# Kernel tuning notes

Hardware: AMD Instinct MI355X
Metric: run time of the kernel (lower is better)

Reference implementation:

```python
import jax, jax.numpy as jnp
import numpy as np

H = 8          # query heads
HKV = 4        # kv heads
D = 256        # head dim
GROUPS = H // HKV
HIDDEN = 2304
WINDOW = 2048  # sliding window
SOFTCAP = 50.0
SCALE = (HIDDEN // H) ** -0.5  # query_pre_attn_scalar uses hidden//heads, not head_dim
NEG = -1e9
ROPE_BASE = 10000.0


def _rope_tables(L, offset=0, dtype=jnp.float32):
    inv_freq = 1.0 / (ROPE_BASE ** (jnp.arange(0, D, 2, dtype=jnp.float32) / D))
    t = jnp.arange(offset, offset + L, dtype=jnp.float32)
    freqs = jnp.outer(t, inv_freq)                    # [L, D/2]
    emb = jnp.concatenate([freqs, freqs], axis=-1)    # [L, D]
    return jnp.cos(emb).astype(dtype), jnp.sin(emb).astype(dtype)


def _rotate_half(x):
    x1, x2 = jnp.split(x, 2, axis=-1)
    return jnp.concatenate([-x2, x1], axis=-1)


def _apply_rope(x, cos, sin):
    # x: [B, h, L, D]; cos/sin: [L, D]
    return x * cos[None, None] + _rotate_half(x) * sin[None, None]


def setup_inputs() -> dict:
    key = jax.random.key(0)
    ks = jax.random.split(key, 5)
    B, L = 1, 4096
    x = jax.random.normal(ks[0], (B, L, HIDDEN), dtype=jnp.float32)
    wq = jax.random.normal(ks[1], (HIDDEN, H * D), dtype=jnp.float32) * 0.02
    wk = jax.random.normal(ks[2], (HIDDEN, HKV * D), dtype=jnp.float32) * 0.02
    wv = jax.random.normal(ks[3], (HIDDEN, HKV * D), dtype=jnp.float32) * 0.02
    wo = jax.random.normal(ks[4], (H * D, HIDDEN), dtype=jnp.float32) * 0.02
    # additive causal mask [1,1,L,L]
    causal = jnp.triu(jnp.full((L, L), NEG, dtype=jnp.float32), k=1)
    mask = causal[None, None]
    return {"x": x, "mask": mask, "wq": wq, "wk": wk, "wv": wv, "wo": wo}


def reference(x, mask, wq, wk, wv, wo):
    B, L, _ = x.shape
    q = (x @ wq).reshape(B, L, H, D).transpose(0, 2, 1, 3)     # [B,H,L,D]
    k = (x @ wk).reshape(B, L, HKV, D).transpose(0, 2, 1, 3)   # [B,HKV,L,D]
    v = (x @ wv).reshape(B, L, HKV, D).transpose(0, 2, 1, 3)

    cos, sin = _rope_tables(L, 0, q.dtype)
    q = _apply_rope(q, cos, sin)
    k = _apply_rope(k, cos, sin)

    # GQA: repeat_interleave kv heads
    k = jnp.repeat(k, GROUPS, axis=1)  # [B,H,L,D]
    v = jnp.repeat(v, GROUPS, axis=1)

    attn = jnp.einsum("bhqd,bhkd->bhqk", q, k) * SCALE
    attn = SOFTCAP * jnp.tanh(attn / SOFTCAP)
    attn = attn + mask

    kv_len = attn.shape[-1]
    if kv_len > WINDOW:  # sliding branch: keep only last WINDOW key columns
        col_keep = jnp.arange(kv_len) >= (kv_len - WINDOW)  # [kv_len]
        attn = jnp.where(col_keep[None, None, None, :], attn, NEG)

    attn = jax.nn.softmax(attn.astype(jnp.float32), axis=-1).astype(q.dtype)
    out = jnp.einsum("bhqk,bhkd->bhqd", attn, v)
    out = out.transpose(0, 2, 1, 3).reshape(B, L, H * D)
    return out @ wo
```

## Files before the change

kernel.cpp:

```cpp
#include <hip/hip_runtime.h>

typedef unsigned short u16;
typedef __bf16 bf16x8 __attribute__((ext_vector_type(8)));
typedef float floatx4 __attribute__((ext_vector_type(4)));
typedef unsigned short u16x4 __attribute__((ext_vector_type(4)));
typedef unsigned short u16x8 __attribute__((ext_vector_type(8)));

#define L_SEQ 4096
#define HID   2304
#define NH    8
#define NKV   4
#define HD    256
#define QDIM  2048
#define KVDIM 1024
#define SCALE_F 0.05892556509887896f

__device__ __forceinline__ u16 f2bf(float f) {
  unsigned u = __float_as_uint(f);
  u += 0x7FFFu + ((u >> 16) & 1u);
  return (u16)(u >> 16);
}
__device__ __forceinline__ float bf2f(u16 h) {
  return __uint_as_float(((unsigned)h) << 16);
}

__device__ __forceinline__ void async_load16(const u16* g, u16* lds_base) {
  __builtin_amdgcn_global_load_lds(
      (const __attribute__((address_space(1))) unsigned int*)g,
      (__attribute__((address_space(3))) unsigned int*)lds_base, 16, 0, 0);
}

__global__ __launch_bounds__(256)
void transpose_kernel(const float* __restrict__ wq, const float* __restrict__ wk,
                      const float* __restrict__ wv, const float* __restrict__ wo,
                      const float* __restrict__ x,
                      u16* __restrict__ wqkvT, u16* __restrict__ woT,
                      u16* __restrict__ xb) {
  const int z = blockIdx.z;
  if (z == 4) {
    const int n4 = L_SEQ * HID / 4;
    const int bid = blockIdx.y * 72 + blockIdx.x;
    const int stride = 5184 * 256;
#pragma unroll
    for (int k = 0; k < 2; ++k) {
      const int i = bid * 256 + threadIdx.x + k * stride;
      if (i < n4) {
        float4 v = *reinterpret_cast<const float4*>(&x[(size_t)i * 4]);
        u16x4 o;
        o[0] = f2bf(v.x); o[1] = f2bf(v.y); o[2] = f2bf(v.z); o[3] = f2bf(v.w);
        *reinterpret_cast<u16x4*>(&xb[(size_t)i * 4]) = o;
      }
    }
    return;
  }
  const float* W; u16* WT; int K, N;
  if (z == 0)      { W = wq; WT = wqkvT;                            K = HID;  N = QDIM; }
  else if (z == 1) { W = wk; WT = wqkvT + (size_t)QDIM * HID;       K = HID;  N = KVDIM; }
  else if (z == 2) { W = wv; WT = wqkvT + (size_t)(QDIM + KVDIM) * HID; K = HID; N = KVDIM; }
  else             { W = wo; WT = woT;                              K = QDIM; N = HID; }
  const int n0 = blockIdx.x * 32, k0 = blockIdx.y * 32;
  if (n0 >= N || k0 >= K) return;
  __shared__ u16 t[32][33];
  const int c = threadIdx.x & 31, r4 = (threadIdx.x >> 5) * 4;
#pragma unroll
  for (int i = 0; i < 4; ++i)
    t[r4 + i][c] = f2bf(W[(size_t)(k0 + r4 + i) * N + n0 + c]);
  __syncthreads();
  const int nn = threadIdx.x & 31, kb = (threadIdx.x >> 5) * 4;
  u16x4 o;
#pragma unroll
  for (int j = 0; j < 4; ++j) o[j] = t[kb + j][nn];
  *reinterpret_cast<u16x4*>(&WT[(size_t)(n0 + nn) * K + k0 + kb]) = o;
}

#define G256_NT 36

#define G256_BARRIER() __builtin_amdgcn_s_barrier()
#define G256_SCHEDB()  __builtin_amdgcn_sched_barrier(0)

#define G256_STAGE(bb, X, kh, tt)                                              \
  {                                                                            \
    const u16* g = (X) ? BT + (size_t)(n0 + w * 32 + srow) * HID               \
                       : A + (size_t)(m0 + w * 32 + srow) * HID;               \
    const int kc = (tt) * 64 + (kh) * 32 + schk;                               \
    async_load16(g + kc, &lds[bb][X][kh][(w * 32) * 32]);                      \
    async_load16(g + 16 * HID + kc, &lds[bb][X][kh][(w * 32 + 16) * 32]);      \
  }

#define G256_RD_B(dst, bb, kk)                                                 \
  {                                                                            \
    const u16* Bk = &lds[bb][1][kk][0];                                        \
    _Pragma("unroll") for (int nt = 0; nt < 4; ++nt)                           \
        dst[nt] = *reinterpret_cast<const bf16x8*>(                            \
            &Bk[(wn + nt * 16 + l16) * 32 + rsw]);                             \
  }

#define G256_RD_A(dst, bb, kk, ch)                                             \
  {                                                                            \
    const u16* Ak = &lds[bb][0][kk][0];                                        \
    _Pragma("unroll") for (int mt = 0; mt < 4; ++mt)                           \
        dst[mt] = *reinterpret_cast<const bf16x8*>(                            \
            &Ak[(wm + ((ch) * 4 + mt) * 16 + l16) * 32 + rsw]);                \
  }

#define G256_MFMA(ch, AA, BB)                                                  \
  {                                                                            \
    __builtin_amdgcn_s_setprio(1);                                             \
    _Pragma("unroll") for (int mt = 0; mt < 4; ++mt)                           \
        _Pragma("unroll") for (int nt = 0; nt < 4; ++nt)                       \
            acc[(ch) * 4 + mt][nt] = __builtin_amdgcn_mfma_f32_16x16x32_bf16(  \
                AA[mt], BB[nt], acc[(ch) * 4 + mt][nt], 0, 0, 0);              \
    __builtin_amdgcn_s_setprio(0);                                             \
  }

#define G256_VMCNT4() __asm__ volatile("s_waitcnt vmcnt(4)")
#define G256_VMCNT0() __asm__ volatile("s_waitcnt vmcnt(0)")

__global__ __launch_bounds__(512)
void gemm256_kernel(const u16* __restrict__ A, const u16* __restrict__ BT,
                    u16* __restrict__ C) {
  __shared__ __align__(16) u16 lds[2][2][2][256 * 32];

  const int tid  = threadIdx.x;
  const int lane = tid & 63;
  const int w    = tid >> 6;
  const int l16  = lane & 15;
  const int quad = lane >> 4;
  const int wm   = (w >> 2) * 128;
  const int wn   = (w & 3) * 64;

  const int srow = lane >> 2;
  const int schk = (((lane & 3) ^ ((lane >> 3) & 3))) * 8;
  const int rsw = ((quad ^ ((l16 >> 1) & 3))) * 8;

  const int bid = blockIdx.x;
  const int id  = (bid & 7) * 20 + (bid >> 3);

  int m0, n0, region;
  if (id < 64)      { region = 0; n0 = (id & 7) * 256;          m0 = 2048 + (id >> 3) * 256; }
  else if (id < 96) { region = 1; const int i = id - 64;
                      n0 = 2048 + (i & 3) * 256;                m0 = 2048 + (i >> 2) * 256; }
  else              { region = 2; const int i = id - 96;
                      n0 = 3072 + (i & 3) * 256;                m0 = (i >> 2) * 256; }

  floatx4 acc[8][4];
#pragma unroll
  for (int i = 0; i < 8; ++i)
#pragma unroll
    for (int j = 0; j < 4; ++j) acc[i][j] = (floatx4){0.f, 0.f, 0.f, 0.f};

  G256_STAGE(0, 0, 0, 0); G256_STAGE(0, 1, 0, 0);
  G256_STAGE(0, 0, 1, 0); G256_STAGE(0, 1, 1, 0);
  G256_STAGE(1, 0, 0, 1); G256_STAGE(1, 1, 0, 1);
  G256_VMCNT4();
  G256_BARRIER();

#pragma unroll 2
  for (int t = 0; t < G256_NT; ++t) {
    const int bb = t & 1;
    bf16x8 a_cur[4], b_cur[4], a_hi0[4], a_lo1[4], b1[4], a_hi1[4];

    G256_RD_A(a_cur, bb, 0, 0);
    G256_RD_B(b_cur, bb, 0);
    G256_RD_A(a_hi0, bb, 0, 1);
    if (t + 1 < G256_NT) { G256_STAGE(bb ^ 1, 0, 1, t + 1); }
    G256_SCHEDB();
    G256_MFMA(0, a_cur, b_cur);
    G256_BARRIER();

    G256_RD_A(a_lo1, bb, 1, 0);
    G256_RD_B(b1, bb, 1);
    if (t + 1 < G256_NT) { G256_STAGE(bb ^ 1, 1, 1, t + 1); }
    G256_SCHEDB();
    G256_MFMA(1, a_hi0, b_cur);
    G256_BARRIER();

    G256_RD_A(a_hi1, bb, 1, 1);
    if (t + 2 < G256_NT) { G256_STAGE(bb, 0, 0, t + 2); }
    G256_SCHEDB();
    G256_MFMA(0, a_lo1, b1);
    G256_BARRIER();

    if (t + 2 < G256_NT) { G256_STAGE(bb, 1, 0, t + 2); }
    G256_SCHEDB();
    G256_MFMA(1, a_hi1, b1);
    if (t < G256_NT - 2) { G256_VMCNT4(); }
    else                 { G256_VMCNT0(); }
    G256_BARRIER();
  }

#pragma unroll
  for (int mt = 0; mt < 8; ++mt)
#pragma unroll
    for (int nt = 0; nt < 4; ++nt) {
      const int mbase = m0 + wm + mt * 16 + quad * 4;
      const int n = n0 + wn + nt * 16 + l16;
      if (region == 0) {
        const size_t base = (size_t)(n >> 8) * L_SEQ * HD + (n & 255);
#pragma unroll
        for (int r = 0; r < 4; ++r)
          C[base + (size_t)(mbase + r) * HD] = f2bf(acc[mt][nt][r] * SCALE_F);
      } else if (region == 1) {
        const int nk2 = n - QDIM;
        const size_t base = (size_t)NH * L_SEQ * HD +
                            (size_t)(nk2 >> 8) * L_SEQ * HD + (nk2 & 255);
#pragma unroll
        for (int r = 0; r < 4; ++r)
          C[base + (size_t)(mbase + r) * HD] = f2bf(acc[mt][nt][r]);
      } else {
        const int nv = n - QDIM - KVDIM;
        u16x4 o;
#pragma unroll
        for (int r = 0; r < 4; ++r) o[r] = f2bf(acc[mt][nt][r]);
        *reinterpret_cast<u16x4*>(
            &C[(size_t)(NH + NKV) * L_SEQ * HD +
               ((size_t)(nv >> 8) * HD + (nv & 255)) * L_SEQ + mbase]) = o;
      }
    }
}

#define GOUT_NT 32

#define GP_STAGE(KS, bb, X, kh, tt)                                            \
  {                                                                            \
    const u16* g = (X) ? BT + (size_t)(n0 + w * 32 + srow) * (KS)              \
                       : A + (size_t)(m0 + w * 32 + srow) * (KS);              \
    const int kc = (tt) * 64 + (kh) * 32 + schk;                               \
    async_load16(g + kc, &lds[bb][X][kh][(w * 32) * 32]);                      \
    async_load16(g + 16 * (KS) + kc, &lds[bb][X][kh][(w * 32 + 16) * 32]);     \
  }

#define GP_RD(dstA, dstB, bb, kk)                                              \
  {                                                                            \
    const u16* Ak = &lds[bb][0][kk][0];                                        \
    const u16* Bk = &lds[bb][1][kk][0];                                        \
    _Pragma("unroll") for (int mt = 0; mt < 4; ++mt)                           \
        dstA[mt] = *reinterpret_cast<const bf16x8*>(                           \
            &Ak[(wm + mt * 16 + l16) * 32 + rsw]);                             \
    _Pragma("unroll") for (int nt = 0; nt < 4; ++nt)                           \
        dstB[nt] = *reinterpret_cast<const bf16x8*>(                           \
            &Bk[(wn + nt * 16 + l16) * 32 + rsw]);                             \
  }

#define GP_MFMA(AA, BB)                                                        \
  {                                                                            \
    __builtin_amdgcn_s_setprio(1);                                             \
    _Pragma("unroll") for (int mt = 0; mt < 4; ++mt)                           \
        _Pragma("unroll") for (int nt = 0; nt < 4; ++nt)                       \
            acc[mt][nt] = __builtin_amdgcn_mfma_f32_16x16x32_bf16(             \
                AA[mt], BB[nt], acc[mt][nt], 0, 0, 0);                         \
    __builtin_amdgcn_s_setprio(0);                                             \
  }

__global__ __launch_bounds__(256)
void gemm_out_kernel(const u16* __restrict__ A, const u16* __restrict__ BT,
                     float* __restrict__ C, const float* __restrict__ rvec,
                     float* __restrict__ out_lo) {
  __shared__ __align__(16) u16 lds[2][2][2][128 * 32];

  const int bid = blockIdx.x;
  const int id  = (bid & 7) * 45 + (bid >> 3);

  if (id >= 288) {
    const int b = id - 288;
    const int total = 2048 * 576;
    for (int i = b * 256 + threadIdx.x; i < total; i += 72 * 256) {
      const int col4 = i % 576;
      *reinterpret_cast<float4*>(&out_lo[(size_t)i * 4]) =
          *reinterpret_cast<const float4*>(&rvec[col4 * 4]);
    }
    return;
  }

  const int tid  = threadIdx.x;
  const int lane = tid & 63;
  const int w    = tid >> 6;
  const int l16  = lane & 15;
  const int quad = lane >> 4;
  const int wm   = (w >> 1) * 64;
  const int wn   = (w & 1) * 64;

  const int srow = lane >> 2;
  const int schk = (((lane & 3) ^ ((lane >> 3) & 3))) * 8;
  const int rsw  = ((quad ^ ((l16 >> 1) & 3))) * 8;

  const int n0  = (id % 18) * 128;
  const int m0  = (id / 18) * 128;

  floatx4 acc[4][4];
#pragma unroll
  for (int i = 0; i < 4; ++i)
#pragma unroll
    for (int j = 0; j < 4; ++j) acc[i][j] = (floatx4){0.f, 0.f, 0.f, 0.f};

  GP_STAGE(QDIM, 0, 0, 0, 0); GP_STAGE(QDIM, 0, 1, 0, 0);
  GP_STAGE(QDIM, 0, 0, 1, 0); GP_STAGE(QDIM, 0, 1, 1, 0);
  GP_STAGE(QDIM, 1, 0, 0, 1); GP_STAGE(QDIM, 1, 1, 0, 1);
  G256_VMCNT4();
  G256_BARRIER();

#pragma unroll 2
  for (int t = 0; t < GOUT_NT; ++t) {
    const int bb = t & 1;
    bf16x8 a0[4], b0[4], a1[4], b1[4];

    GP_RD(a0, b0, bb, 0);
    GP_RD(a1, b1, bb, 1);
    if (t + 1 < GOUT_NT) { GP_STAGE(QDIM, bb ^ 1, 0, 1, t + 1);
                           GP_STAGE(QDIM, bb ^ 1, 1, 1, t + 1); }
    G256_SCHEDB();
    GP_MFMA(a0, b0);
    G256_BARRIER();

    if (t + 2 < GOUT_NT) { GP_STAGE(QDIM, bb, 0, 0, t + 2);
                           GP_STAGE(QDIM, bb, 1, 0, t + 2); }
    G256_SCHEDB();
    GP_MFMA(a1, b1);
    if (t < GOUT_NT - 2) { G256_VMCNT4(); }
    else                 { G256_VMCNT0(); }
    G256_BARRIER();
  }

#pragma unroll
  for (int mt = 0; mt < 4; ++mt)
#pragma unroll
    for (int nt = 0; nt < 4; ++nt) {
      const int mbase = m0 + wm + mt * 16 + quad * 4;
      const int n = n0 + wn + nt * 16 + l16;
#pragma unroll
      for (int r = 0; r < 4; ++r)
        C[(size_t)(mbase + r) * HID + n] = acc[mt][nt][r];
    }
}

__global__ __launch_bounds__(384)
void rope_meanv_kernel(u16* __restrict__ qb, u16* __restrict__ kb,
                       const u16* __restrict__ vt, float* __restrict__ mv) {
  if (blockIdx.x >= 2048) {
    if (threadIdx.x >= 256) return;
    const int row  = (blockIdx.x - 2048) * 4 + (threadIdx.x >> 6);
    const int lane = threadIdx.x & 63;
    const u16* p = vt + (size_t)row * L_SEQ;
    float s = 0.f;
#pragma unroll
    for (int c = 0; c < 8; ++c) {
      u16x8 v = *reinterpret_cast<const u16x8*>(&p[(c * 64 + lane) * 8]);
#pragma unroll
      for (int j = 0; j < 8; ++j) s += bf2f(v[j]);
    }
#pragma unroll
    for (int off = 32; off > 0; off >>= 1) s += __shfl_xor(s, off, 64);
    if (lane == 0) mv[row] = s * (1.0f / 4096.0f);
    return;
  }
  const int l  = 2048 + blockIdx.x;
  const int hh = threadIdx.x >> 5;
  const int d0 = (threadIdx.x & 31) * 4;
  u16* base = (hh < NH) ? qb + ((size_t)hh * L_SEQ + l) * HD
                        : kb + ((size_t)(hh - NH) * L_SEQ + l) * HD;
  u16x4 x1v = *reinterpret_cast<const u16x4*>(&base[d0]);
  u16x4 x2v = *reinterpret_cast<const u16x4*>(&base[d0 + 128]);
  u16x4 o1, o2;
#pragma unroll
  for (int i = 0; i < 4; ++i) {
    const float invf = exp2f((float)(d0 + i) * (-13.287712379549449f / 128.0f));
    const float ang = (float)l * invf;
    float s, c;
    sincosf(ang, &s, &c);
    const float x1 = bf2f(x1v[i]);
    const float x2 = bf2f(x2v[i]);
    o1[i] = f2bf(x1 * c - x2 * s);
    o2[i] = f2bf(x2 * c + x1 * s);
  }
  *reinterpret_cast<u16x4*>(&base[d0])       = o1;
  *reinterpret_cast<u16x4*>(&base[d0 + 128]) = o2;
}

__global__ __launch_bounds__(256)
void rowvec_part_kernel(const float* __restrict__ mv, const float* __restrict__ wo,
                        float* __restrict__ rpart) {
  const int j = blockIdx.x * 256 + threadIdx.x;
  const int c0 = blockIdx.y * 128;
  float acc = 0.f;
#pragma unroll 4
  for (int cc = 0; cc < 128; ++cc) {
    const int c = c0 + cc;
    const float a = mv[((c >> 9) << 8) | (c & 255)];
    acc += a * wo[(size_t)c * HID + j];
  }
  rpart[blockIdx.y * HID + j] = acc;
}

__global__ __launch_bounds__(256)
void rowvec_reduce_kernel(const float* __restrict__ rpart, float* __restrict__ r) {
  const int j = blockIdx.x * 256 + threadIdx.x;
  float s = 0.f;
#pragma unroll
  for (int p = 0; p < 16; ++p) s += rpart[p * HID + j];
  r[j] = s;
}

#define ATT_STAGE(g_, buf_)                                                    \
  {                                                                            \
    const int kt_ = r_off[run] + (g_);                                         \
    const u16* kg_ = kg0 + (size_t)kt_ * 32 * HD;                              \
    _Pragma("unroll") for (int p_ = 0; p_ < 4; ++p_) {                         \
      const int r_   = w * 8 + p_ * 2 + (lane >> 5);                           \
      const int pos_ = lane & 31;                                              \
      const int c_   = (pos_ & 24) | ((pos_ ^ r_) & 7);                        \
      async_load16(&kg_[(size_t)r_ * HD + c_ * 8],                             \
                   &Klds[buf_][(w * 8 + p_ * 2) * 256]);                       \
    }                                                                          \
    const u16* vg_ = vg0 + kt_ * 32;                                           \
    _Pragma("unroll") for (int j_ = 0; j_ < 4; ++j_) {                         \
      const int m_  = w * 32 + j_ * 8 + (lane >> 3);                           \
      const int p2_ = lane & 7;                                                \
      const int c2_ = p2_ ^ (m_ & 7);                                          \
      const int r2_ = m_ * 2 + (c2_ >> 2);                                     \
      async_load16(&vg_[(size_t)r2_ * L_SEQ + (c2_ & 3) * 8],                  \
                   &Vlds[buf_][(w * 32 + j_ * 8) * 64]);                       \
    }                                                                          \
  }

__global__ __launch_bounds__(256)
void attn_kernel(const u16* __restrict__ qb, const u16* __restrict__ kb,
                 const u16* __restrict__ vt, u16* __restrict__ Opart,
                 float* __restrict__ lpart) {
  const int s = blockIdx.x;
  const int pr = blockIdx.y;
  const int h = blockIdx.z;
  const int kvh = h >> 1;
  const int tid = threadIdx.x;
  const int w = tid >> 6, lane = tid & 63;
  const int l16 = lane & 15, quad = lane >> 4;

  __shared__ __align__(16) u16 Klds[2][32 * 256];
  __shared__ __align__(16) u16 Vlds[2][256 * 32];
  __shared__ u16 Plds[4][16][40];

  const int n_a = 2 * pr + 2;
  const int lo = (66 * s) >> 2;
  const int hi = (66 * (s + 1)) >> 2;

  const int r_lo[2] = {lo, (lo > n_a) ? lo : n_a};
  const int r_hi[2] = {(hi < n_a) ? hi : n_a, hi};
  const int r_t[2]  = {32 + pr, 63 - pr};
  const int r_off[2] = {64, 64 - n_a};

  const u16* kg0 = kb + (size_t)kvh * L_SEQ * HD;
  const u16* vg0 = vt + (size_t)kvh * HD * L_SEQ;

  for (int run = 0; run < 2; ++run) {
    if (r_lo[run] >= r_hi[run]) continue;
    const int t  = r_t[run];
    const int q0 = t * 64 + w * 16;
    const int glo = r_lo[run], ghi = r_hi[run];

    bf16x8 aq[8];
    {
      const u16* qr = qb + ((size_t)h * L_SEQ + q0 + l16) * HD + quad * 8;
#pragma unroll
      for (int f = 0; f < 8; ++f)
        aq[f] = *reinterpret_cast<const bf16x8*>(&qr[f * 32]);
#pragma unroll
      for (int f = 0; f < 8; ++f) {
        floatx4& t4 = reinterpret_cast<floatx4&>(aq[f]);
        __asm__ volatile("" : "+v"(t4));
      }
    }

    ATT_STAGE(glo, 0);
    if (glo + 1 < ghi) ATT_STAGE(glo + 1, 1);

    floatx4 acc[16];
#pragma unroll
    for (int i = 0; i < 16; ++i) acc[i] = (floatx4){0.f, 0.f, 0.f, 0.f};
    float lsum[4] = {0.f, 0.f, 0.f, 0.f};

    for (int g = glo; g < ghi; ++g) {
      const int cur = (g - glo) & 1;
      const int kt = r_off[run] + g;
      if (g + 1 < ghi) { __asm__ volatile("s_waitcnt vmcnt(8)"); }
      else             { __asm__ volatile("s_waitcnt vmcnt(0)"); }
      __builtin_amdgcn_s_barrier();

      const u16* Kb = &Klds[cur][0];
      const u16* Vb = &Vlds[cur][0];

      floatx4 sa[2] = {(floatx4){0.f, 0.f, 0.f, 0.f}, (floatx4){0.f, 0.f, 0.f, 0.f}};
#pragma unroll
      for (int nt = 0; nt < 2; ++nt) {
        const int row = nt * 16 + l16;
#pragma unroll
        for (int f = 0; f < 8; ++f) {
          const int c   = f * 4 + quad;
          const int pos = (c & 24) | ((c ^ row) & 7);
          bf16x8 bk = *reinterpret_cast<const bf16x8*>(&Kb[row * 256 + pos * 8]);
          sa[nt] = __builtin_amdgcn_mfma_f32_16x16x32_bf16(aq[f], bk, sa[nt], 0, 0, 0);
        }
      }
#pragma unroll
      for (int nt = 0; nt < 2; ++nt) {
        const int key = kt * 32 + nt * 16 + l16;
#pragma unroll
        for (int r = 0; r < 4; ++r) {
          const float x = sa[nt][r];
          const float capm50 = -100.0f / (__expf(x * 0.04f) + 1.0f);
          float p = __expf(capm50);
          const int qq = q0 + quad * 4 + r;
          p = (key <= qq) ? p : 0.0f;
          lsum[r] += p;
          Plds[w][quad * 4 + r][nt * 16 + l16] = f2bf(p);
        }
      }
      bf16x8 ap = *reinterpret_cast<const bf16x8*>(&Plds[w][l16][quad * 8]);
#pragma unroll
      for (int dt = 0; dt < 16; ++dt) {
        const int rV = dt * 16 + l16;
        const int m  = rV >> 1;
        const int p  = ((rV & 1) * 4 + quad) ^ (m & 7);
        bf16x8 bv = *reinterpret_cast<const bf16x8*>(&Vb[m * 64 + p * 8]);
        acc[dt] = __builtin_amdgcn_mfma_f32_16x16x32_bf16(ap, bv, acc[dt], 0, 0, 0);
      }

      __builtin_amdgcn_s_barrier();
      if (g + 2 < ghi) ATT_STAGE(g + 2, cur);
    }

#pragma unroll
    for (int r = 0; r < 4; ++r) {
      float l = lsum[r];
      l += __shfl_xor(l, 1); l += __shfl_xor(l, 2);
      l += __shfl_xor(l, 4); l += __shfl_xor(l, 8);
      lsum[r] = l;
    }
    const int ql0 = q0 - 2048 + quad * 4;
#pragma unroll
    for (int r = 0; r < 4; ++r) {
      u16* orow = Opart + (((size_t)s * NH + h) * 2048 + ql0 + r) * HD + l16;
#pragma unroll
      for (int dt = 0; dt < 16; ++dt) orow[dt * 16] = f2bf(acc[dt][r]);
      if (l16 == 0) lpart[((size_t)s * NH + h) * 2048 + ql0 + r] = lsum[r];
    }
  }
}

__global__ __launch_bounds__(256)
void combine_kernel(const u16* __restrict__ Opart, const float* __restrict__ lpart,
                    u16* __restrict__ ab) {
  const int idx4 = blockIdx.x * 256 + threadIdx.x;
  const int d4 = (idx4 & 63) * 4;
  const int ql = (idx4 >> 6) & 2047;
  const int h  = idx4 >> 17;
  const int qtile = ql >> 6;
  const bool role_a = qtile < 16;
  const int pr = role_a ? qtile : 31 - qtile;
  const int lo_s[4] = {0, 16, 33, 49};
  const int hi_s[4] = {16, 33, 49, 66};

  float4 o = {0.f, 0.f, 0.f, 0.f};
  float l = 0.f;
#pragma unroll
  for (int s = 0; s < 4; ++s) {
    const bool valid = role_a ? (lo_s[s] < 2 * pr + 2) : (hi_s[s] > 2 * pr + 2);
    if (valid) {
      u16x4 v = *reinterpret_cast<const u16x4*>(
          &Opart[(((size_t)s * NH + h) * 2048 + ql) * HD + d4]);
      o.x += bf2f(v[0]); o.y += bf2f(v[1]); o.z += bf2f(v[2]); o.w += bf2f(v[3]);
      l += lpart[((size_t)s * NH + h) * 2048 + ql];
    }
  }
  const float inv = 1.0f / l;
  u16x4 ov;
  ov[0] = f2bf(o.x * inv); ov[1] = f2bf(o.y * inv);
  ov[2] = f2bf(o.z * inv); ov[3] = f2bf(o.w * inv);
  *reinterpret_cast<u16x4*>(&ab[(size_t)(2048 + ql) * QDIM + h * HD + d4]) = ov;
}

extern "C" void kernel_launch(void* const* d_in, const int* in_sizes, int n_in,
                              void* d_out, int out_size, void* d_ws, size_t ws_size,
                              hipStream_t stream) {
  const float* x  = (const float*)d_in[0];
  const float* wq = (const float*)d_in[2];
  const float* wk = (const float*)d_in[3];
  const float* wv = (const float*)d_in[4];
  const float* wo = (const float*)d_in[5];
  float* out = (float*)d_out;

  u16* qb  = (u16*)d_ws;
  u16* kb  = qb  + (size_t)NH  * L_SEQ * HD;
  u16* vtb = kb  + (size_t)NKV * L_SEQ * HD;
  u16* ab  = vtb + (size_t)NKV * L_SEQ * HD;
  u16* xb  = ab  + (size_t)L_SEQ * QDIM;
  u16* wqkvT = xb + (size_t)L_SEQ * HID;
  u16* woT = wqkvT + (size_t)(QDIM + 2 * KVDIM) * HID;
  u16* Opart = woT + (size_t)HID * QDIM;
  float* lpart = (float*)(Opart + (size_t)4 * NH * 2048 * HD);
  float* mv    = lpart + (size_t)4 * NH * 2048;
  float* rpart = mv + 1024;
  float* rvec  = rpart + 16 * HID;

  transpose_kernel<<<dim3(72, 72, 5), 256, 0, stream>>>(
      wq, wk, wv, wo, x, wqkvT, woT, xb);

  gemm256_kernel<<<dim3(160), 512, 0, stream>>>(xb, wqkvT, qb);

  rope_meanv_kernel<<<dim3(2048 + 256), 384, 0, stream>>>(qb, kb, vtb, mv);

  rowvec_part_kernel<<<dim3(9, 16), 256, 0, stream>>>(mv, wo, rpart);
  rowvec_reduce_kernel<<<dim3(9), 256, 0, stream>>>(rpart, rvec);

  attn_kernel<<<dim3(4, 16, NH), 256, 0, stream>>>(qb, kb, vtb, Opart, lpart);
  combine_kernel<<<dim3(4096), 256, 0, stream>>>(Opart, lpart, ab);

  gemm_out_kernel<<<dim3(360), 256, 0, stream>>>(
      ab + (size_t)2048 * QDIM, woT, out + (size_t)2048 * HID, rvec, out);
}
```

Before: 328.6 us.

## Single-buffer V in LDS and split attention work into six KV chunks

V tiles now go into a single LDS buffer, loaded right after the compute barrier, while K stays double-buffered. This cuts LDS per block so more blocks can be resident. The KV range per pair is now split into six chunks of 11 tiles instead of four, giving 768 blocks instead of 512 for better CU fill. The cost is exposed V load latency, more partial outputs written to workspace, and more reads in the combine kernel.

```diff
diff --git a/kernel.cpp b/kernel.cpp
--- a/kernel.cpp
+++ b/kernel.cpp
@@ -400,7 +400,7 @@
   r[j] = s;
 }
 
-#define ATT_STAGE(g_, buf_)                                                    \
+#define ATT_STAGE_K(g_, buf_)                                                  \
   {                                                                            \
     const int kt_ = r_off[run] + (g_);                                         \
     const u16* kg_ = kg0 + (size_t)kt_ * 32 * HD;                              \
@@ -411,6 +411,11 @@
       async_load16(&kg_[(size_t)r_ * HD + c_ * 8],                             \
                    &Klds[buf_][(w * 8 + p_ * 2) * 256]);                       \
     }                                                                          \
+  }
+
+#define ATT_STAGE_V(g_)                                                        \
+  {                                                                            \
+    const int kt_ = r_off[run] + (g_);                                         \
     const u16* vg_ = vg0 + kt_ * 32;                                           \
     _Pragma("unroll") for (int j_ = 0; j_ < 4; ++j_) {                         \
       const int m_  = w * 32 + j_ * 8 + (lane >> 3);                           \
@@ -418,7 +423,7 @@
       const int c2_ = p2_ ^ (m_ & 7);                                          \
       const int r2_ = m_ * 2 + (c2_ >> 2);                                     \
       async_load16(&vg_[(size_t)r2_ * L_SEQ + (c2_ & 3) * 8],                  \
-                   &Vlds[buf_][(w * 32 + j_ * 8) * 64]);                       \
+                   &Vlds[(w * 32 + j_ * 8) * 64]);                             \
     }                                                                          \
   }
 
@@ -435,12 +440,12 @@
   const int l16 = lane & 15, quad = lane >> 4;
 
   __shared__ __align__(16) u16 Klds[2][32 * 256];
-  __shared__ __align__(16) u16 Vlds[2][256 * 32];
+  __shared__ __align__(16) u16 Vlds[256 * 32];
   __shared__ u16 Plds[4][16][40];
 
   const int n_a = 2 * pr + 2;
-  const int lo = (66 * s) >> 2;
-  const int hi = (66 * (s + 1)) >> 2;
+  const int lo = 11 * s;
+  const int hi = 11 * (s + 1);
 
   const int r_lo[2] = {lo, (lo > n_a) ? lo : n_a};
   const int r_hi[2] = {(hi < n_a) ? hi : n_a, hi};
@@ -469,8 +474,9 @@
       }
     }
 
-    ATT_STAGE(glo, 0);
-    if (glo + 1 < ghi) ATT_STAGE(glo + 1, 1);
+    ATT_STAGE_K(glo, 0);
+    ATT_STAGE_V(glo);
+    if (glo + 1 < ghi) ATT_STAGE_K(glo + 1, 1);
 
     floatx4 acc[16];
 #pragma unroll
@@ -480,12 +486,11 @@
     for (int g = glo; g < ghi; ++g) {
       const int cur = (g - glo) & 1;
       const int kt = r_off[run] + g;
-      if (g + 1 < ghi) { __asm__ volatile("s_waitcnt vmcnt(8)"); }
+      if (g + 1 < ghi) { __asm__ volatile("s_waitcnt vmcnt(4)"); }
       else             { __asm__ volatile("s_waitcnt vmcnt(0)"); }
       __builtin_amdgcn_s_barrier();
 
       const u16* Kb = &Klds[cur][0];
-      const u16* Vb = &Vlds[cur][0];
 
       floatx4 sa[2] = {(floatx4){0.f, 0.f, 0.f, 0.f}, (floatx4){0.f, 0.f, 0.f, 0.f}};
 #pragma unroll
@@ -519,12 +524,13 @@
         const int rV = dt * 16 + l16;
         const int m  = rV >> 1;
         const int p  = ((rV & 1) * 4 + quad) ^ (m & 7);
-        bf16x8 bv = *reinterpret_cast<const bf16x8*>(&Vb[m * 64 + p * 8]);
+        bf16x8 bv = *reinterpret_cast<const bf16x8*>(&Vlds[m * 64 + p * 8]);
         acc[dt] = __builtin_amdgcn_mfma_f32_16x16x32_bf16(ap, bv, acc[dt], 0, 0, 0);
       }
 
       __builtin_amdgcn_s_barrier();
-      if (g + 2 < ghi) ATT_STAGE(g + 2, cur);
+      if (g + 1 < ghi) ATT_STAGE_V(g + 1);
+      if (g + 2 < ghi) ATT_STAGE_K(g + 2, cur);
     }
 
 #pragma unroll
@@ -555,14 +561,13 @@
   const int qtile = ql >> 6;
   const bool role_a = qtile < 16;
   const int pr = role_a ? qtile : 31 - qtile;
-  const int lo_s[4] = {0, 16, 33, 49};
-  const int hi_s[4] = {16, 33, 49, 66};
+  const int n_a = 2 * pr + 2;
 
   float4 o = {0.f, 0.f, 0.f, 0.f};
   float l = 0.f;
 #pragma unroll
-  for (int s = 0; s < 4; ++s) {
-    const bool valid = role_a ? (lo_s[s] < 2 * pr + 2) : (hi_s[s] > 2 * pr + 2);
+  for (int s = 0; s < 6; ++s) {
+    const bool valid = role_a ? (11 * s < n_a) : (11 * s + 11 > n_a);
     if (valid) {
       u16x4 v = *reinterpret_cast<const u16x4*>(
           &Opart[(((size_t)s * NH + h) * 2048 + ql) * HD + d4]);
@@ -595,8 +600,8 @@
   u16* wqkvT = xb + (size_t)L_SEQ * HID;
   u16* woT = wqkvT + (size_t)(QDIM + 2 * KVDIM) * HID;
   u16* Opart = woT + (size_t)HID * QDIM;
-  float* lpart = (float*)(Opart + (size_t)4 * NH * 2048 * HD);
-  float* mv    = lpart + (size_t)4 * NH * 2048;
+  float* lpart = (float*)(Opart + (size_t)6 * NH * 2048 * HD);
+  float* mv    = lpart + (size_t)6 * NH * 2048;
   float* rpart = mv + 1024;
   float* rvec  = rpart + 16 * HID;
 
@@ -610,7 +615,7 @@
   rowvec_part_kernel<<<dim3(9, 16), 256, 0, stream>>>(mv, wo, rpart);
   rowvec_reduce_kernel<<<dim3(9), 256, 0, stream>>>(rpart, rvec);
 
-  attn_kernel<<<dim3(4, 16, NH), 256, 0, stream>>>(qb, kb, vtb, Opart, lpart);
+  attn_kernel<<<dim3(6, 16, NH), 256, 0, stream>>>(qb, kb, vtb, Opart, lpart);
   combine_kernel<<<dim3(4096), 256, 0, stream>>>(Opart, lpart, ab);
 
   gemm_out_kernel<<<dim3(360), 256, 0, stream>>>(
```

Result: slower. 340.2 us (+3.5%).
